# Performance work log

Hardware: AMD Instinct MI355X
Metric: run time of the kernel (lower is better)

The kernel has to match this reference:

```python
import jax, jax.numpy as jnp
import numpy as np

N = 100000   # nodes
E = 600000   # edges (no self loops by construction)
F = 64       # feature_size
H = 2 * F    # hidden_size = 128
G = 32       # graphs in batch
L = N // G   # nodes per graph (equal-size graphs)
NEG_SLOPE = 0.2  # GATConv default leaky_relu slope


def setup_inputs() -> dict:
    key = jax.random.key(0)
    ks = jax.random.split(key, 16)
    x = jax.random.normal(ks[0], (N, F), jnp.float32)
    # edges guaranteed to have no self loops (PyG GAT removes then re-adds them)
    src = jax.random.randint(ks[1], (E,), 0, N)
    off = jax.random.randint(ks[2], (E,), 1, N)
    dst = (src + off) % N
    edge_index = jnp.stack([src, dst]).astype(jnp.int32)
    batch = (jnp.arange(N) // L).astype(jnp.int32)
    sF = 1.0 / np.sqrt(F)
    sH = 1.0 / np.sqrt(H)
    return {
        "x": x, "edge_index": edge_index, "batch": batch,
        "W0": jax.random.normal(ks[3], (F, H), jnp.float32) * sF,
        "b0": jnp.zeros((H,), jnp.float32),
        "Wg": jax.random.normal(ks[4], (H, H), jnp.float32) * sH,
        "att_src": jax.random.normal(ks[5], (H,), jnp.float32) * sH,
        "att_dst": jax.random.normal(ks[6], (H,), jnp.float32) * sH,
        "W1": jax.random.normal(ks[7], (H, H), jnp.float32) * sH,
        "b1": jnp.zeros((H,), jnp.float32),
        "W2": jax.random.normal(ks[8], (H, H), jnp.float32) * sH,
        "b2": jnp.zeros((H,), jnp.float32),
        "Wr": jax.random.normal(ks[9], (H, F), jnp.float32) * sH,
        "br": jnp.zeros((F,), jnp.float32),
    }


def _gcn(x, row, col, w, W, b):
    # PyG GCNConv (normalize=True); edges already include self loops, w holds edge weights.
    xw = x @ W
    deg = jax.ops.segment_sum(w, col, num_segments=N)
    dinv = jnp.where(deg > 0, deg, 1.0) ** -0.5
    dinv = jnp.where(deg > 0, dinv, 0.0)
    norm = dinv[row] * w * dinv[col]                      # [E+N]
    out = jax.ops.segment_sum(xw[row] * norm[:, None], col, num_segments=N)
    return out + b


def reference(x, edge_index, batch, W0, b0, Wg, att_src, att_dst, W1, b1, W2, b2, Wr, br):
    row, col = edge_index[0], edge_index[1]
    loops = jnp.arange(N, dtype=edge_index.dtype)
    row_f = jnp.concatenate([row, loops])                 # [E+N] with self loops
    col_f = jnp.concatenate([col, loops])

    # initial GCNConv (gcn_norm adds self loops with weight 1) + relu
    x = jax.nn.relu(_gcn(x, row_f, col_f, jnp.ones(E + N, x.dtype), W0, b0))

    # GATConv attention (heads=1); node output is discarded in the torch module
    xg = x @ Wg
    a_s = xg @ att_src
    a_d = xg @ att_dst
    e = jax.nn.leaky_relu(a_s[row_f] + a_d[col_f], NEG_SLOPE)
    m = jax.ops.segment_max(e, col_f, num_segments=N)
    ex = jnp.exp(e - m[col_f])
    alpha = ex / jax.ops.segment_sum(ex, col_f, num_segments=N)[col_f]

    # gcn_norm's add_remaining_self_loops replaces self-loop weights with 1.0
    w = alpha.at[E:].set(1.0)

    x = jax.nn.relu(_gcn(x, row_f, col_f, w, W1, b1))
    x = jax.nn.relu(_gcn(x, row_f, col_f, w, W2, b2))

    # readout: Dropout (eval -> identity) + Linear
    out = x @ Wr + br                                     # [N, F]

    # unbatch + pad_sequence (batch_first=True); batch ids are sorted
    counts = jax.ops.segment_sum(jnp.ones(N, jnp.int32), batch, num_segments=G)
    starts = jnp.concatenate([jnp.zeros(1, jnp.int32), jnp.cumsum(counts)[:-1].astype(jnp.int32)])
    pos = jnp.arange(N, dtype=jnp.int32) - starts[batch]
    emb = jnp.zeros((G, L, F), out.dtype).at[batch, pos].set(out)
    return emb
```

## Files before the change

kernel.cpp:

```cpp
#include <hip/hip_runtime.h>
#include <hip/hip_bf16.h>
#include <math.h>

#define NN 100000
#define EE 600000
#define FF 64
#define HH 128
#define CHUNK 1024
#define NCHUNK ((NN + CHUNK - 1) / CHUNK)
#define NCHUNKS_M (NN / 16)

typedef unsigned short u16;
typedef __attribute__((ext_vector_type(8))) short bf16x8;
typedef __attribute__((ext_vector_type(4))) float f32x4;

__device__ __forceinline__ u16 f2bf(float f) {
    __hip_bfloat16 h = __float2bfloat16(f);
    return *(u16*)&h;
}
__device__ __forceinline__ float bf2f(u16 u) {
    unsigned int t = ((unsigned int)u) << 16;
    return *(float*)&t;
}


__global__ void count_k(const int* __restrict__ col, int* __restrict__ cnt) {
    int e = blockIdx.x * 256 + threadIdx.x;
    if (e < EE) atomicAdd(&cnt[col[e]], 1);
}

__global__ void dinv1_k(const int* __restrict__ cnt, float* __restrict__ dinv1) {
    int c = blockIdx.x * 256 + threadIdx.x;
    if (c < NN) dinv1[c] = rsqrtf((float)cnt[c] + 1.0f);
}

__global__ void chunksum_k(const int* __restrict__ cnt, int* __restrict__ chunk_sum) {
    int b = blockIdx.x, t = threadIdx.x;
    int base = b * CHUNK + t * 4;
    int s = 0;
    #pragma unroll
    for (int i = 0; i < 4; i++) { int idx = base + i; if (idx < NN) s += cnt[idx]; }
    __shared__ int sm[4];
    for (int d = 32; d > 0; d >>= 1) s += __shfl_down(s, d);
    if ((t & 63) == 0) sm[t >> 6] = s;
    __syncthreads();
    if (t == 0) chunk_sum[b] = sm[0] + sm[1] + sm[2] + sm[3];
}

__global__ void chunkoff_k(const int* __restrict__ chunk_sum, int* __restrict__ chunk_off,
                           int* __restrict__ col_ptr) {
    if (threadIdx.x == 0) {
        int run = 0;
        for (int i = 0; i < NCHUNK; i++) { chunk_off[i] = run; run += chunk_sum[i]; }
        col_ptr[NN] = run;
    }
}

__global__ void colptr_k(const int* __restrict__ cnt, const int* __restrict__ chunk_off,
                         int* __restrict__ col_ptr) {
    int b = blockIdx.x, t = threadIdx.x;
    int base = b * CHUNK + t * 4;
    int c[4]; int tot = 0;
    #pragma unroll
    for (int i = 0; i < 4; i++) { int idx = base + i; c[i] = (idx < NN) ? cnt[idx] : 0; tot += c[i]; }
    __shared__ int s[256];
    s[t] = tot;
    __syncthreads();
    for (int d = 1; d < 256; d <<= 1) {
        int v = (t >= d) ? s[t - d] : 0;
        __syncthreads();
        s[t] += v;
        __syncthreads();
    }
    int excl = s[t] - tot;
    int off = chunk_off[b] + excl;
    int pre = 0;
    #pragma unroll
    for (int i = 0; i < 4; i++) {
        int idx = base + i;
        if (idx < NN) col_ptr[idx] = off + pre;
        pre += c[i];
    }
}

__global__ void fill_k(const int* __restrict__ row, const int* __restrict__ col,
                       const int* __restrict__ col_ptr, int* __restrict__ cursor,
                       const float* __restrict__ dinv1, int* __restrict__ csr_src,
                       float* __restrict__ csr_w) {
    int e = blockIdx.x * 256 + threadIdx.x;
    if (e < EE) {
        int r = row[e], c = col[e];
        int slot = col_ptr[c] + atomicAdd(&cursor[c], 1);
        csr_src[slot] = r;
        csr_w[slot] = dinv1[r] * dinv1[c];
    }
}


__global__ void cast_k(const float* __restrict__ x, u16* __restrict__ xb) {
    int i = blockIdx.x * 256 + threadIdx.x;
    if (i < NN * FF / 4) {
        float4 v = ((const float4*)x)[i];
        ushort4 o;
        o.x = f2bf(v.x); o.y = f2bf(v.y); o.z = f2bf(v.z); o.w = f2bf(v.w);
        ((ushort4*)xb)[i] = o;
    }
}


__global__ void gemv_vsvd_k(const float* __restrict__ Wg, const float* __restrict__ att_src,
                            const float* __restrict__ att_dst, float* __restrict__ vs,
                            float* __restrict__ vd) {
    int i = threadIdx.x;
    if (i < HH) {
        float s1 = 0.f, s2 = 0.f;
        for (int j = 0; j < HH; j++) {
            float w = Wg[i * HH + j];
            s1 += w * att_src[j];
            s2 += w * att_dst[j];
        }
        vs[i] = s1;
        vd[i] = s2;
    }
}


__global__ void prep_wt_k(const float* __restrict__ W0, const float* __restrict__ W1,
                          const float* __restrict__ W2, const float* __restrict__ Wr,
                          u16* __restrict__ Wt0, u16* __restrict__ Wt1,
                          u16* __restrict__ Wt2, u16* __restrict__ Wtr) {
    int i = blockIdx.x * 256 + threadIdx.x;
    if (i < 8192) {
        int n = i >> 6, k = i & 63;
        Wt0[i] = f2bf(W0[k * 128 + n]);
        return;
    }
    i -= 8192;
    if (i < 16384) {
        int n = i >> 7, k = i & 127;
        Wt1[i] = f2bf(W1[k * 128 + n]);
        return;
    }
    i -= 16384;
    if (i < 16384) {
        int n = i >> 7, k = i & 127;
        Wt2[i] = f2bf(W2[k * 128 + n]);
        return;
    }
    i -= 16384;
    if (i < 8192) {
        int n = i >> 7, k = i & 127;
        Wtr[i] = f2bf(Wr[k * 64 + n]);
    }
}


__global__ __launch_bounds__(256) void aggx_k(
    const u16* __restrict__ xb, const int* __restrict__ col_ptr, const int* __restrict__ csr_src,
    const float* __restrict__ csr_w, const float* __restrict__ dinv1, u16* __restrict__ xout) {
    int wid = threadIdx.x >> 6, lane = threadIdx.x & 63;
    int c = blockIdx.x * 4 + wid;
    if (c >= NN) return;
    int q = lane >> 4;
    int ch = (lane & 15) << 2;
    int beg = col_ptr[c], end = col_ptr[c + 1];
    float4 acc = make_float4(0.f, 0.f, 0.f, 0.f);

    int pA = beg + q, pB = pA + 4;
    int rA = 0, rB = 0; float wA = 0.f, wB = 0.f;
    if (pA < end) { rA = csr_src[pA]; wA = csr_w[pA]; }
    if (pB < end) { rB = csr_src[pB]; wB = csr_w[pB]; }
    while (pA < end) {
        bool hb = pB < end;
        ushort4 vA = *(const ushort4*)&xb[(size_t)rA * FF + ch];
        ushort4 vB;
        if (hb) vB = *(const ushort4*)&xb[(size_t)rB * FF + ch];
        int pA2 = pA + 8, pB2 = pB + 8;
        int rA2 = 0, rB2 = 0; float wA2 = 0.f, wB2 = 0.f;
        if (pA2 < end) { rA2 = csr_src[pA2]; wA2 = csr_w[pA2]; }
        if (pB2 < end) { rB2 = csr_src[pB2]; wB2 = csr_w[pB2]; }
        acc.x += bf2f(vA.x) * wA;
        acc.y += bf2f(vA.y) * wA;
        acc.z += bf2f(vA.z) * wA;
        acc.w += bf2f(vA.w) * wA;
        if (hb) {
            acc.x += bf2f(vB.x) * wB;
            acc.y += bf2f(vB.y) * wB;
            acc.z += bf2f(vB.z) * wB;
            acc.w += bf2f(vB.w) * wB;
        }
        pA = pA2; pB = pB2; rA = rA2; rB = rB2; wA = wA2; wB = wB2;
    }
    acc.x += __shfl_xor(acc.x, 16); acc.y += __shfl_xor(acc.y, 16);
    acc.z += __shfl_xor(acc.z, 16); acc.w += __shfl_xor(acc.w, 16);
    acc.x += __shfl_xor(acc.x, 32); acc.y += __shfl_xor(acc.y, 32);
    acc.z += __shfl_xor(acc.z, 32); acc.w += __shfl_xor(acc.w, 32);

    if (q == 0) {
        ushort4 v = *(const ushort4*)&xb[(size_t)c * FF + ch];
        float dc = dinv1[c];
        float ws = dc * dc;
        acc.x = fmaf(bf2f(v.x), ws, acc.x);
        acc.y = fmaf(bf2f(v.y), ws, acc.y);
        acc.z = fmaf(bf2f(v.z), ws, acc.z);
        acc.w = fmaf(bf2f(v.w), ws, acc.w);
        ushort4 o;
        o.x = f2bf(acc.x); o.y = f2bf(acc.y); o.z = f2bf(acc.z); o.w = f2bf(acc.w);
        *(ushort4*)&xout[(size_t)c * FF + ch] = o;
    }
}


__global__ __launch_bounds__(256) void gemm1_k(const u16* __restrict__ A, const u16* __restrict__ Wt,
                                               const float* __restrict__ bias,
                                               const float* __restrict__ vs, const float* __restrict__ vd,
                                               u16* __restrict__ C, float* __restrict__ a_s,
                                               float* __restrict__ a_d) {
    constexpr int K = FF, N = HH, KK = K / 32, NT = N / 16;
    int lane = threadIdx.x & 63;
    int l15 = lane & 15, l4 = lane >> 4;
    int wg = blockIdx.x * 4 + (threadIdx.x >> 6);
    int nwaves = gridDim.x * 4;

    bf16x8 a_frag[KK][NT];
    #pragma unroll
    for (int kk = 0; kk < KK; kk++)
        #pragma unroll
        for (int nt = 0; nt < NT; nt++)
            a_frag[kk][nt] = *(const bf16x8*)&Wt[(size_t)(nt * 16 + l15) * K + kk * 32 + l4 * 8];
    f32x4 bias_f[NT], vs_f[NT], vd_f[NT];
    #pragma unroll
    for (int nt = 0; nt < NT; nt++) {
        bias_f[nt] = *(const f32x4*)&bias[nt * 16 + l4 * 4];
        vs_f[nt] = *(const f32x4*)&vs[nt * 16 + l4 * 4];
        vd_f[nt] = *(const f32x4*)&vd[nt * 16 + l4 * 4];
    }

    for (int ch = wg; ch < NCHUNKS_M; ch += nwaves) {
        int row = ch * 16 + l15;
        bf16x8 b_frag[KK];
        #pragma unroll
        for (int kk = 0; kk < KK; kk++)
            b_frag[kk] = *(const bf16x8*)&A[(size_t)row * K + kk * 32 + l4 * 8];
        f32x4 acc[NT] = {};
        #pragma unroll
        for (int kk = 0; kk < KK; kk++)
            #pragma unroll
            for (int nt = 0; nt < NT; nt++)
                acc[nt] = __builtin_amdgcn_mfma_f32_16x16x32_bf16(a_frag[kk][nt], b_frag[kk],
                                                                  acc[nt], 0, 0, 0);
        float s1 = 0.f, s2 = 0.f;
        #pragma unroll
        for (int nt = 0; nt < NT; nt++) {
            float o0 = fmaxf(acc[nt][0] + bias_f[nt][0], 0.f);
            float o1 = fmaxf(acc[nt][1] + bias_f[nt][1], 0.f);
            float o2 = fmaxf(acc[nt][2] + bias_f[nt][2], 0.f);
            float o3 = fmaxf(acc[nt][3] + bias_f[nt][3], 0.f);
            ushort4 o;
            o.x = f2bf(o0); o.y = f2bf(o1); o.z = f2bf(o2); o.w = f2bf(o3);
            *(ushort4*)&C[(size_t)row * N + nt * 16 + l4 * 4] = o;
            s1 += o0 * vs_f[nt][0] + o1 * vs_f[nt][1] + o2 * vs_f[nt][2] + o3 * vs_f[nt][3];
            s2 += o0 * vd_f[nt][0] + o1 * vd_f[nt][1] + o2 * vd_f[nt][2] + o3 * vd_f[nt][3];
        }
        s1 += __shfl_xor(s1, 16); s1 += __shfl_xor(s1, 32);
        s2 += __shfl_xor(s2, 16); s2 += __shfl_xor(s2, 32);
        if (l4 == 0) {
            a_s[row] = s1;
            a_d[row] = s2;
        }
    }
}


template <int K, int N, bool OUTF32>
__global__ __launch_bounds__(256) void mfma_gemm_k(const u16* __restrict__ A,
                                                   const u16* __restrict__ Wt,
                                                   const float* __restrict__ bias,
                                                   void* __restrict__ C_) {
    constexpr int KK = K / 32;
    constexpr int NT = N / 16;
    int lane = threadIdx.x & 63;
    int l15 = lane & 15, l4 = lane >> 4;
    int wg = blockIdx.x * 4 + (threadIdx.x >> 6);
    int nwaves = gridDim.x * 4;

    bf16x8 a_frag[KK][NT];
    #pragma unroll
    for (int kk = 0; kk < KK; kk++)
        #pragma unroll
        for (int nt = 0; nt < NT; nt++)
            a_frag[kk][nt] = *(const bf16x8*)&Wt[(size_t)(nt * 16 + l15) * K + kk * 32 + l4 * 8];

    f32x4 bias_f[NT];
    if (OUTF32) {
        #pragma unroll
        for (int nt = 0; nt < NT; nt++)
            bias_f[nt] = *(const f32x4*)&bias[nt * 16 + l4 * 4];
    }

    float* Cf = (float*)C_;
    u16* Cb = (u16*)C_;

    for (int ch = wg; ch < NCHUNKS_M; ch += nwaves) {
        int row = ch * 16 + l15;
        bf16x8 b_frag[KK];
        #pragma unroll
        for (int kk = 0; kk < KK; kk++)
            b_frag[kk] = *(const bf16x8*)&A[(size_t)row * K + kk * 32 + l4 * 8];
        f32x4 acc[NT] = {};
        #pragma unroll
        for (int kk = 0; kk < KK; kk++)
            #pragma unroll
            for (int nt = 0; nt < NT; nt++)
                acc[nt] = __builtin_amdgcn_mfma_f32_16x16x32_bf16(a_frag[kk][nt], b_frag[kk],
                                                                  acc[nt], 0, 0, 0);
        #pragma unroll
        for (int nt = 0; nt < NT; nt++) {
            int col = nt * 16 + l4 * 4;
            if (OUTF32) {
                float4 o;
                o.x = acc[nt][0] + bias_f[nt][0];
                o.y = acc[nt][1] + bias_f[nt][1];
                o.z = acc[nt][2] + bias_f[nt][2];
                o.w = acc[nt][3] + bias_f[nt][3];
                *(float4*)&Cf[(size_t)row * N + col] = o;
            } else {
                ushort4 o;
                o.x = f2bf(acc[nt][0]);
                o.y = f2bf(acc[nt][1]);
                o.z = f2bf(acc[nt][2]);
                o.w = f2bf(acc[nt][3]);
                *(ushort4*)&Cb[(size_t)row * N + col] = o;
            }
        }
    }
}


__global__ __launch_bounds__(256) void attn_k(const int* __restrict__ col_ptr,
                                              const int* __restrict__ csr_src,
                                              const float* __restrict__ a_s,
                                              const float* __restrict__ a_d,
                                              float* __restrict__ alpha,
                                              float* __restrict__ dinv2) {
    int lane = threadIdx.x & 63, wid = threadIdx.x >> 6;
    int grp = lane >> 3, idx = lane & 7;
    int c = blockIdx.x * 32 + wid * 8 + grp;
    if (c >= NN) return;
    int beg = col_ptr[c], end = col_ptr[c + 1];
    float ad = a_d[c];
    float es = a_s[c] + ad;
    es = (es > 0.f) ? es : 0.2f * es;
    float m = (idx == 0) ? es : -1e30f;
    float s = (idx == 0) ? 1.f : 0.f;
    for (int p = beg + idx; p < end; p += 8) {
        float e = a_s[csr_src[p]] + ad;
        e = (e > 0.f) ? e : 0.2f * e;
        alpha[p] = e;
        float mn = fmaxf(m, e);
        s = s * expf(m - mn) + expf(e - mn);
        m = mn;
    }
    #pragma unroll
    for (int d = 1; d < 8; d <<= 1) {
        float mo = __shfl_xor(m, d);
        float so = __shfl_xor(s, d);
        float mn = fmaxf(m, mo);
        s = s * expf(m - mn) + so * expf(mo - mn);
        m = mn;
    }
    float inv = 1.f / s;
    float aself = expf(es - m) * inv;
    float d2 = rsqrtf(2.f - aself);
    if (idx == 0) dinv2[c] = d2;
    float sc = inv * d2;
    for (int p = beg + idx; p < end; p += 8)
        alpha[p] = expf(alpha[p] - m) * sc;
}

__global__ void w2_k(const int* __restrict__ csr_src, const float* __restrict__ dinv2,
                     float* __restrict__ alpha) {
    int p = blockIdx.x * 256 + threadIdx.x;
    if (p < EE) alpha[p] *= dinv2[csr_src[p]];
}


__global__ __launch_bounds__(256) void agg2_k(
    const u16* __restrict__ xw, const int* __restrict__ col_ptr, const int* __restrict__ csr_src,
    const float* __restrict__ w2, const float* __restrict__ dinv2, const float* __restrict__ bias,
    u16* __restrict__ xout) {
    int wid = threadIdx.x >> 6, lane = threadIdx.x & 63;
    int c = blockIdx.x * 4 + wid;
    if (c >= NN) return;
    int half = lane >> 5;
    int ch = (lane & 31) << 2;
    int beg = col_ptr[c], end = col_ptr[c + 1];
    float4 acc = make_float4(0.f, 0.f, 0.f, 0.f);

    int pA = beg + half, pB = pA + 2, pC = pA + 4;
    int rA = 0, rB = 0, rC = 0; float wA = 0.f, wB = 0.f, wC = 0.f;
    if (pA < end) { rA = csr_src[pA]; wA = w2[pA]; }
    if (pB < end) { rB = csr_src[pB]; wB = w2[pB]; }
    if (pC < end) { rC = csr_src[pC]; wC = w2[pC]; }
    while (pA < end) {
        bool hb = pB < end, hc = pC < end;
        ushort4 vA = *(const ushort4*)&xw[(size_t)rA * HH + ch];
        ushort4 vB, vC;
        if (hb) vB = *(const ushort4*)&xw[(size_t)rB * HH + ch];
        if (hc) vC = *(const ushort4*)&xw[(size_t)rC * HH + ch];
        int pA2 = pA + 6, pB2 = pB + 6, pC2 = pC + 6;
        int rA2 = 0, rB2 = 0, rC2 = 0; float wA2 = 0.f, wB2 = 0.f, wC2 = 0.f;
        if (pA2 < end) { rA2 = csr_src[pA2]; wA2 = w2[pA2]; }
        if (pB2 < end) { rB2 = csr_src[pB2]; wB2 = w2[pB2]; }
        if (pC2 < end) { rC2 = csr_src[pC2]; wC2 = w2[pC2]; }
        acc.x += bf2f(vA.x) * wA;
        acc.y += bf2f(vA.y) * wA;
        acc.z += bf2f(vA.z) * wA;
        acc.w += bf2f(vA.w) * wA;
        if (hb) {
            acc.x += bf2f(vB.x) * wB;
            acc.y += bf2f(vB.y) * wB;
            acc.z += bf2f(vB.z) * wB;
            acc.w += bf2f(vB.w) * wB;
        }
        if (hc) {
            acc.x += bf2f(vC.x) * wC;
            acc.y += bf2f(vC.y) * wC;
            acc.z += bf2f(vC.z) * wC;
            acc.w += bf2f(vC.w) * wC;
        }
        pA = pA2; pB = pB2; pC = pC2;
        rA = rA2; rB = rB2; rC = rC2;
        wA = wA2; wB = wB2; wC = wC2;
    }
    acc.x += __shfl_xor(acc.x, 32);
    acc.y += __shfl_xor(acc.y, 32);
    acc.z += __shfl_xor(acc.z, 32);
    acc.w += __shfl_xor(acc.w, 32);

    if (half == 0) {
        ushort4 v = *(const ushort4*)&xw[(size_t)c * HH + ch];
        float dc = dinv2[c];
        float ws = dc * dc;
        float4 b4 = *(const float4*)&bias[ch];
        acc.x = fmaxf(fmaf(bf2f(v.x), ws, acc.x) + b4.x, 0.f);
        acc.y = fmaxf(fmaf(bf2f(v.y), ws, acc.y) + b4.y, 0.f);
        acc.z = fmaxf(fmaf(bf2f(v.z), ws, acc.z) + b4.z, 0.f);
        acc.w = fmaxf(fmaf(bf2f(v.w), ws, acc.w) + b4.w, 0.f);
        ushort4 o;
        o.x = f2bf(acc.x); o.y = f2bf(acc.y); o.z = f2bf(acc.z); o.w = f2bf(acc.w);
        *(ushort4*)&xout[(size_t)c * HH + ch] = o;
    }
}


extern "C" void kernel_launch(void* const* d_in, const int* in_sizes, int n_in,
                              void* d_out, int out_size, void* d_ws, size_t ws_size,
                              hipStream_t stream) {
    const float* x = (const float*)d_in[0];
    const int* eidx = (const int*)d_in[1];
    const float* W0 = (const float*)d_in[3];
    const float* b0 = (const float*)d_in[4];
    const float* Wg = (const float*)d_in[5];
    const float* att_src = (const float*)d_in[6];
    const float* att_dst = (const float*)d_in[7];
    const float* W1 = (const float*)d_in[8];
    const float* b1 = (const float*)d_in[9];
    const float* W2 = (const float*)d_in[10];
    const float* b2 = (const float*)d_in[11];
    const float* Wr = (const float*)d_in[12];
    const float* br = (const float*)d_in[13];
    float* out = (float*)d_out;

    const int* erow = eidx;
    const int* ecol = eidx + EE;

    char* p = (char*)d_ws;
    auto alloc = [&](size_t bytes) {
        void* r = (void*)p;
        p += (bytes + 255) & ~(size_t)255;
        return r;
    };
    int* col_ptr = (int*)alloc((NN + 1) * sizeof(int));
    int* csr_src = (int*)alloc(EE * sizeof(int));
    float* csr_w = (float*)alloc(EE * sizeof(float));
    int* cnt = (int*)alloc(NN * sizeof(int));
    int* cursor = (int*)alloc(NN * sizeof(int));
    int* chunk_sum = (int*)alloc(128 * sizeof(int));
    int* chunk_off = (int*)alloc(128 * sizeof(int));
    float* alpha = (float*)alloc(EE * sizeof(float));
    float* dinv1 = (float*)alloc(NN * sizeof(float));
    float* dinv2 = (float*)alloc(NN * sizeof(float));
    float* a_s = (float*)alloc(NN * sizeof(float));
    float* a_d = (float*)alloc(NN * sizeof(float));
    float* vs = (float*)alloc(HH * sizeof(float));
    float* vd = (float*)alloc(HH * sizeof(float));
    u16* Wt0 = (u16*)alloc(8192 * sizeof(u16));
    u16* Wt1 = (u16*)alloc(16384 * sizeof(u16));
    u16* Wt2 = (u16*)alloc(16384 * sizeof(u16));
    u16* Wtr = (u16*)alloc(8192 * sizeof(u16));
    u16* xb = (u16*)alloc((size_t)NN * FF * sizeof(u16));
    u16* xaggb = (u16*)alloc((size_t)NN * FF * sizeof(u16));
    u16* bufA = (u16*)alloc((size_t)NN * HH * sizeof(u16));
    u16* bufB = (u16*)alloc((size_t)NN * HH * sizeof(u16));

    hipMemsetAsync(cnt, 0, NN * sizeof(int), stream);
    hipMemsetAsync(cursor, 0, NN * sizeof(int), stream);

    count_k<<<(EE + 255) / 256, 256, 0, stream>>>(ecol, cnt);
    dinv1_k<<<(NN + 255) / 256, 256, 0, stream>>>(cnt, dinv1);
    chunksum_k<<<NCHUNK, 256, 0, stream>>>(cnt, chunk_sum);
    chunkoff_k<<<1, 64, 0, stream>>>(chunk_sum, chunk_off, col_ptr);
    colptr_k<<<NCHUNK, 256, 0, stream>>>(cnt, chunk_off, col_ptr);
    fill_k<<<(EE + 255) / 256, 256, 0, stream>>>(erow, ecol, col_ptr, cursor, dinv1,
                                                 csr_src, csr_w);
    cast_k<<<(NN * FF / 4 + 255) / 256, 256, 0, stream>>>(x, xb);
    gemv_vsvd_k<<<1, 128, 0, stream>>>(Wg, att_src, att_dst, vs, vd);
    prep_wt_k<<<192, 256, 0, stream>>>(W0, W1, W2, Wr, Wt0, Wt1, Wt2, Wtr);

    int aggGrid = (NN + 3) / 4;
    const int GG = 512;

    aggx_k<<<aggGrid, 256, 0, stream>>>(xb, col_ptr, csr_src, csr_w, dinv1, xaggb);
    gemm1_k<<<GG, 256, 0, stream>>>(xaggb, Wt0, b0, vs, vd, bufA, a_s, a_d);
    attn_k<<<(NN + 31) / 32, 256, 0, stream>>>(col_ptr, csr_src, a_s, a_d, alpha, dinv2);
    w2_k<<<(EE + 255) / 256, 256, 0, stream>>>(csr_src, dinv2, alpha);
    mfma_gemm_k<HH, HH, false><<<GG, 256, 0, stream>>>(bufA, Wt1, nullptr, bufB);
    agg2_k<<<aggGrid, 256, 0, stream>>>(bufB, col_ptr, csr_src, alpha, dinv2, b1, bufA);
    mfma_gemm_k<HH, HH, false><<<GG, 256, 0, stream>>>(bufA, Wt2, nullptr, bufB);
    agg2_k<<<aggGrid, 256, 0, stream>>>(bufB, col_ptr, csr_src, alpha, dinv2, b2, bufA);
    mfma_gemm_k<HH, FF, true><<<GG, 256, 0, stream>>>(bufA, Wtr, br, out);
}
```

Baseline: 279.3 us.

## Merge small setup kernels and interleave CSR source and weight into int2

Folds the dinv1 computation into chunksum_k, seeds the fill cursor with absolute column offsets in colptr_k (dropping a memset and one col_ptr read per edge), and merges the x cast, weight transposes and the vs/vd GEMV into one prep kernel. CSR source index and edge weight are packed as int2 (meta1 for the first layer, meta2 for the two later layers), so each aggregation gather reads one 8-byte load instead of two separate arrays. This cuts launch count and metadata loads at the cost of two extra 4.8 MB int2 arrays. The GEMV now runs inside a large grid's tail block, so it no longer runs alone in its own one-block launch.

```diff
diff --git a/kernel.cpp b/kernel.cpp
--- a/kernel.cpp
+++ b/kernel.cpp
@@ -29,17 +29,20 @@
     if (e < EE) atomicAdd(&cnt[col[e]], 1);
 }
 
-__global__ void dinv1_k(const int* __restrict__ cnt, float* __restrict__ dinv1) {
-    int c = blockIdx.x * 256 + threadIdx.x;
-    if (c < NN) dinv1[c] = rsqrtf((float)cnt[c] + 1.0f);
-}
-
-__global__ void chunksum_k(const int* __restrict__ cnt, int* __restrict__ chunk_sum) {
+__global__ void chunksum_k(const int* __restrict__ cnt, int* __restrict__ chunk_sum,
+                           float* __restrict__ dinv1) {
     int b = blockIdx.x, t = threadIdx.x;
     int base = b * CHUNK + t * 4;
     int s = 0;
     #pragma unroll
-    for (int i = 0; i < 4; i++) { int idx = base + i; if (idx < NN) s += cnt[idx]; }
+    for (int i = 0; i < 4; i++) {
+        int idx = base + i;
+        if (idx < NN) {
+            int cv = cnt[idx];
+            s += cv;
+            dinv1[idx] = rsqrtf((float)cv + 1.0f);
+        }
+    }
     __shared__ int sm[4];
     for (int d = 32; d > 0; d >>= 1) s += __shfl_down(s, d);
     if ((t & 63) == 0) sm[t >> 6] = s;
@@ -57,7 +60,7 @@
 }
 
 __global__ void colptr_k(const int* __restrict__ cnt, const int* __restrict__ chunk_off,
-                         int* __restrict__ col_ptr) {
+                         int* __restrict__ col_ptr, int* __restrict__ cursor) {
     int b = blockIdx.x, t = threadIdx.x;
     int base = b * CHUNK + t * 4;
     int c[4]; int tot = 0;
@@ -78,40 +81,69 @@
     #pragma unroll
     for (int i = 0; i < 4; i++) {
         int idx = base + i;
-        if (idx < NN) col_ptr[idx] = off + pre;
+        if (idx < NN) {
+            col_ptr[idx] = off + pre;
+            cursor[idx] = off + pre;
+        }
         pre += c[i];
     }
 }
 
 __global__ void fill_k(const int* __restrict__ row, const int* __restrict__ col,
-                       const int* __restrict__ col_ptr, int* __restrict__ cursor,
-                       const float* __restrict__ dinv1, int* __restrict__ csr_src,
-                       float* __restrict__ csr_w) {
+                       int* __restrict__ cursor, const float* __restrict__ dinv1,
+                       int* __restrict__ csr_src, int2* __restrict__ meta1) {
     int e = blockIdx.x * 256 + threadIdx.x;
     if (e < EE) {
         int r = row[e], c = col[e];
-        int slot = col_ptr[c] + atomicAdd(&cursor[c], 1);
+        int slot = atomicAdd(&cursor[c], 1);
         csr_src[slot] = r;
-        csr_w[slot] = dinv1[r] * dinv1[c];
-    }
-}
-
-
-__global__ void cast_k(const float* __restrict__ x, u16* __restrict__ xb) {
+        float w = dinv1[r] * dinv1[c];
+        meta1[slot] = make_int2(r, __float_as_int(w));
+    }
+}
+
+
+__global__ void prep_k(const float* __restrict__ W0, const float* __restrict__ W1,
+                       const float* __restrict__ W2, const float* __restrict__ Wr,
+                       const float* __restrict__ Wg, const float* __restrict__ att_src,
+                       const float* __restrict__ att_dst, const float* __restrict__ x,
+                       u16* __restrict__ Wt0, u16* __restrict__ Wt1,
+                       u16* __restrict__ Wt2, u16* __restrict__ Wtr,
+                       float* __restrict__ vs, float* __restrict__ vd,
+                       u16* __restrict__ xb) {
     int i = blockIdx.x * 256 + threadIdx.x;
     if (i < NN * FF / 4) {
         float4 v = ((const float4*)x)[i];
         ushort4 o;
         o.x = f2bf(v.x); o.y = f2bf(v.y); o.z = f2bf(v.z); o.w = f2bf(v.w);
         ((ushort4*)xb)[i] = o;
-    }
-}
-
-
-__global__ void gemv_vsvd_k(const float* __restrict__ Wg, const float* __restrict__ att_src,
-                            const float* __restrict__ att_dst, float* __restrict__ vs,
-                            float* __restrict__ vd) {
-    int i = threadIdx.x;
+        return;
+    }
+    i -= NN * FF / 4;
+    if (i < 8192) {
+        int n = i >> 6, k = i & 63;
+        Wt0[i] = f2bf(W0[k * 128 + n]);
+        return;
+    }
+    i -= 8192;
+    if (i < 16384) {
+        int n = i >> 7, k = i & 127;
+        Wt1[i] = f2bf(W1[k * 128 + n]);
+        return;
+    }
+    i -= 16384;
+    if (i < 16384) {
+        int n = i >> 7, k = i & 127;
+        Wt2[i] = f2bf(W2[k * 128 + n]);
+        return;
+    }
+    i -= 16384;
+    if (i < 8192) {
+        int n = i >> 7, k = i & 127;
+        Wtr[i] = f2bf(Wr[k * 64 + n]);
+        return;
+    }
+    i -= 8192;
     if (i < HH) {
         float s1 = 0.f, s2 = 0.f;
         for (int j = 0; j < HH; j++) {
@@ -125,39 +157,9 @@
 }
 
 
-__global__ void prep_wt_k(const float* __restrict__ W0, const float* __restrict__ W1,
-                          const float* __restrict__ W2, const float* __restrict__ Wr,
-                          u16* __restrict__ Wt0, u16* __restrict__ Wt1,
-                          u16* __restrict__ Wt2, u16* __restrict__ Wtr) {
-    int i = blockIdx.x * 256 + threadIdx.x;
-    if (i < 8192) {
-        int n = i >> 6, k = i & 63;
-        Wt0[i] = f2bf(W0[k * 128 + n]);
-        return;
-    }
-    i -= 8192;
-    if (i < 16384) {
-        int n = i >> 7, k = i & 127;
-        Wt1[i] = f2bf(W1[k * 128 + n]);
-        return;
-    }
-    i -= 16384;
-    if (i < 16384) {
-        int n = i >> 7, k = i & 127;
-        Wt2[i] = f2bf(W2[k * 128 + n]);
-        return;
-    }
-    i -= 16384;
-    if (i < 8192) {
-        int n = i >> 7, k = i & 127;
-        Wtr[i] = f2bf(Wr[k * 64 + n]);
-    }
-}
-
-
 __global__ __launch_bounds__(256) void aggx_k(
-    const u16* __restrict__ xb, const int* __restrict__ col_ptr, const int* __restrict__ csr_src,
-    const float* __restrict__ csr_w, const float* __restrict__ dinv1, u16* __restrict__ xout) {
+    const u16* __restrict__ xb, const int* __restrict__ col_ptr, const int2* __restrict__ meta1,
+    const float* __restrict__ dinv1, u16* __restrict__ xout) {
     int wid = threadIdx.x >> 6, lane = threadIdx.x & 63;
     int c = blockIdx.x * 4 + wid;
     if (c >= NN) return;
@@ -168,8 +170,8 @@
 
     int pA = beg + q, pB = pA + 4;
     int rA = 0, rB = 0; float wA = 0.f, wB = 0.f;
-    if (pA < end) { rA = csr_src[pA]; wA = csr_w[pA]; }
-    if (pB < end) { rB = csr_src[pB]; wB = csr_w[pB]; }
+    if (pA < end) { int2 m = meta1[pA]; rA = m.x; wA = __int_as_float(m.y); }
+    if (pB < end) { int2 m = meta1[pB]; rB = m.x; wB = __int_as_float(m.y); }
     while (pA < end) {
         bool hb = pB < end;
         ushort4 vA = *(const ushort4*)&xb[(size_t)rA * FF + ch];
@@ -177,8 +179,8 @@
         if (hb) vB = *(const ushort4*)&xb[(size_t)rB * FF + ch];
         int pA2 = pA + 8, pB2 = pB + 8;
         int rA2 = 0, rB2 = 0; float wA2 = 0.f, wB2 = 0.f;
-        if (pA2 < end) { rA2 = csr_src[pA2]; wA2 = csr_w[pA2]; }
-        if (pB2 < end) { rB2 = csr_src[pB2]; wB2 = csr_w[pB2]; }
+        if (pA2 < end) { int2 m = meta1[pA2]; rA2 = m.x; wA2 = __int_as_float(m.y); }
+        if (pB2 < end) { int2 m = meta1[pB2]; rB2 = m.x; wB2 = __int_as_float(m.y); }
         acc.x += bf2f(vA.x) * wA;
         acc.y += bf2f(vA.y) * wA;
         acc.z += bf2f(vA.z) * wA;
@@ -379,16 +381,19 @@
 }
 
 __global__ void w2_k(const int* __restrict__ csr_src, const float* __restrict__ dinv2,
-                     float* __restrict__ alpha) {
+                     const float* __restrict__ alpha, int2* __restrict__ meta2) {
     int p = blockIdx.x * 256 + threadIdx.x;
-    if (p < EE) alpha[p] *= dinv2[csr_src[p]];
+    if (p < EE) {
+        int r = csr_src[p];
+        float w = alpha[p] * dinv2[r];
+        meta2[p] = make_int2(r, __float_as_int(w));
+    }
 }
 
 
 __global__ __launch_bounds__(256) void agg2_k(
-    const u16* __restrict__ xw, const int* __restrict__ col_ptr, const int* __restrict__ csr_src,
-    const float* __restrict__ w2, const float* __restrict__ dinv2, const float* __restrict__ bias,
-    u16* __restrict__ xout) {
+    const u16* __restrict__ xw, const int* __restrict__ col_ptr, const int2* __restrict__ meta2,
+    const float* __restrict__ dinv2, const float* __restrict__ bias, u16* __restrict__ xout) {
     int wid = threadIdx.x >> 6, lane = threadIdx.x & 63;
     int c = blockIdx.x * 4 + wid;
     if (c >= NN) return;
@@ -399,9 +404,9 @@
 
     int pA = beg + half, pB = pA + 2, pC = pA + 4;
     int rA = 0, rB = 0, rC = 0; float wA = 0.f, wB = 0.f, wC = 0.f;
-    if (pA < end) { rA = csr_src[pA]; wA = w2[pA]; }
-    if (pB < end) { rB = csr_src[pB]; wB = w2[pB]; }
-    if (pC < end) { rC = csr_src[pC]; wC = w2[pC]; }
+    if (pA < end) { int2 m = meta2[pA]; rA = m.x; wA = __int_as_float(m.y); }
+    if (pB < end) { int2 m = meta2[pB]; rB = m.x; wB = __int_as_float(m.y); }
+    if (pC < end) { int2 m = meta2[pC]; rC = m.x; wC = __int_as_float(m.y); }
     while (pA < end) {
         bool hb = pB < end, hc = pC < end;
         ushort4 vA = *(const ushort4*)&xw[(size_t)rA * HH + ch];
@@ -410,9 +415,9 @@
         if (hc) vC = *(const ushort4*)&xw[(size_t)rC * HH + ch];
         int pA2 = pA + 6, pB2 = pB + 6, pC2 = pC + 6;
         int rA2 = 0, rB2 = 0, rC2 = 0; float wA2 = 0.f, wB2 = 0.f, wC2 = 0.f;
-        if (pA2 < end) { rA2 = csr_src[pA2]; wA2 = w2[pA2]; }
-        if (pB2 < end) { rB2 = csr_src[pB2]; wB2 = w2[pB2]; }
-        if (pC2 < end) { rC2 = csr_src[pC2]; wC2 = w2[pC2]; }
+        if (pA2 < end) { int2 m = meta2[pA2]; rA2 = m.x; wA2 = __int_as_float(m.y); }
+        if (pB2 < end) { int2 m = meta2[pB2]; rB2 = m.x; wB2 = __int_as_float(m.y); }
+        if (pC2 < end) { int2 m = meta2[pC2]; rC2 = m.x; wC2 = __int_as_float(m.y); }
         acc.x += bf2f(vA.x) * wA;
         acc.y += bf2f(vA.y) * wA;
         acc.z += bf2f(vA.z) * wA;
@@ -483,7 +488,8 @@
     };
     int* col_ptr = (int*)alloc((NN + 1) * sizeof(int));
     int* csr_src = (int*)alloc(EE * sizeof(int));
-    float* csr_w = (float*)alloc(EE * sizeof(float));
+    int2* meta1 = (int2*)alloc(EE * sizeof(int2));
+    int2* meta2 = (int2*)alloc(EE * sizeof(int2));
     int* cnt = (int*)alloc(NN * sizeof(int));
     int* cursor = (int*)alloc(NN * sizeof(int));
     int* chunk_sum = (int*)alloc(128 * sizeof(int));
@@ -505,29 +511,25 @@
     u16* bufB = (u16*)alloc((size_t)NN * HH * sizeof(u16));
 
     hipMemsetAsync(cnt, 0, NN * sizeof(int), stream);
-    hipMemsetAsync(cursor, 0, NN * sizeof(int), stream);
 
     count_k<<<(EE + 255) / 256, 256, 0, stream>>>(ecol, cnt);
-    dinv1_k<<<(NN + 255) / 256, 256, 0, stream>>>(cnt, dinv1);
-    chunksum_k<<<NCHUNK, 256, 0, stream>>>(cnt, chunk_sum);
+    chunksum_k<<<NCHUNK, 256, 0, stream>>>(cnt, chunk_sum, dinv1);
     chunkoff_k<<<1, 64, 0, stream>>>(chunk_sum, chunk_off, col_ptr);
-    colptr_k<<<NCHUNK, 256, 0, stream>>>(cnt, chunk_off, col_ptr);
-    fill_k<<<(EE + 255) / 256, 256, 0, stream>>>(erow, ecol, col_ptr, cursor, dinv1,
-                                                 csr_src, csr_w);
-    cast_k<<<(NN * FF / 4 + 255) / 256, 256, 0, stream>>>(x, xb);
-    gemv_vsvd_k<<<1, 128, 0, stream>>>(Wg, att_src, att_dst, vs, vd);
-    prep_wt_k<<<192, 256, 0, stream>>>(W0, W1, W2, Wr, Wt0, Wt1, Wt2, Wtr);
+    colptr_k<<<NCHUNK, 256, 0, stream>>>(cnt, chunk_off, col_ptr, cursor);
+    fill_k<<<(EE + 255) / 256, 256, 0, stream>>>(erow, ecol, cursor, dinv1, csr_src, meta1);
+    prep_k<<<(NN * FF / 4 + 49280 + 255) / 256, 256, 0, stream>>>(
+        W0, W1, W2, Wr, Wg, att_src, att_dst, x, Wt0, Wt1, Wt2, Wtr, vs, vd, xb);
 
     int aggGrid = (NN + 3) / 4;
     const int GG = 512;
 
-    aggx_k<<<aggGrid, 256, 0, stream>>>(xb, col_ptr, csr_src, csr_w, dinv1, xaggb);
+    aggx_k<<<aggGrid, 256, 0, stream>>>(xb, col_ptr, meta1, dinv1, xaggb);
     gemm1_k<<<GG, 256, 0, stream>>>(xaggb, Wt0, b0, vs, vd, bufA, a_s, a_d);
     attn_k<<<(NN + 31) / 32, 256, 0, stream>>>(col_ptr, csr_src, a_s, a_d, alpha, dinv2);
-    w2_k<<<(EE + 255) / 256, 256, 0, stream>>>(csr_src, dinv2, alpha);
+    w2_k<<<(EE + 255) / 256, 256, 0, stream>>>(csr_src, dinv2, alpha, meta2);
     mfma_gemm_k<HH, HH, false><<<GG, 256, 0, stream>>>(bufA, Wt1, nullptr, bufB);
-    agg2_k<<<aggGrid, 256, 0, stream>>>(bufB, col_ptr, csr_src, alpha, dinv2, b1, bufA);
+    agg2_k<<<aggGrid, 256, 0, stream>>>(bufB, col_ptr, meta2, dinv2, b1, bufA);
     mfma_gemm_k<HH, HH, false><<<GG, 256, 0, stream>>>(bufA, Wt2, nullptr, bufB);
-    agg2_k<<<aggGrid, 256, 0, stream>>>(bufB, col_ptr, csr_src, alpha, dinv2, b2, bufA);
+    agg2_k<<<aggGrid, 256, 0, stream>>>(bufB, col_ptr, meta2, dinv2, b2, bufA);
     mfma_gemm_k<HH, FF, true><<<GG, 256, 0, stream>>>(bufA, Wtr, br, out);
 }
```

New measurement: 297.6 us. 1.07x slower.
